# Optimization experiments

Hardware: AMD Instinct MI355X
Metric: run time of the kernel (lower is better)

The kernel has to match this reference:

```python
import jax, jax.numpy as jnp
import numpy as np

K, D, N = 32, 64, 65536
LOG_2PI = float(np.log(2.0 * np.pi))


def setup_inputs() -> dict:
    key = jax.random.key(0)
    k1, k2, k3, k4 = jax.random.split(key, 4)
    X = jax.random.normal(k1, (N, D), dtype=jnp.float32)
    loc = jax.random.normal(k2, (K, D), dtype=jnp.float32)
    # SPD full covariances per component: A A^T + I
    A = 0.1 * jax.random.normal(k3, (K, D, D), dtype=jnp.float32)
    cov = jnp.einsum('kij,klj->kil', A, A) + jnp.eye(D, dtype=jnp.float32)
    pi = jax.random.normal(k4, (K,), dtype=jnp.float32)
    return {"X": X, "loc": loc, "cov": cov, "pi": pi}


def _gmm_log_prob(X, loc, cov, pi):
    d = X.shape[-1]
    L = jnp.linalg.cholesky(cov)                       # [K, d, d]
    diff = X[:, None, :] - loc[None, :, :]             # [N, K, d]
    # per-component triangular solve: z_k = L_k^{-1} (x - mu_k)
    solve = lambda Lk, dk: jax.scipy.linalg.solve_triangular(Lk, dk.T, lower=True)  # [d, N]
    z = jax.vmap(solve, in_axes=(0, 1))(L, diff)       # [K, d, N]
    maha = jnp.sum(z * z, axis=1).T                    # [N, K]
    half_logdet = jnp.sum(jnp.log(jnp.diagonal(L, axis1=-2, axis2=-1)), axis=-1)  # [K]
    comp_logp = -0.5 * (d * LOG_2PI + maha) - half_logdet[None, :]  # [N, K]
    # Categorical(softmax(pi)).logits followed by log_softmax == log_softmax(pi)
    weighted = comp_logp + jax.nn.log_softmax(pi)[None, :]
    return jax.scipy.special.logsumexp(weighted, axis=1, keepdims=True)  # [N, 1]


def reference(X, loc, cov, pi):
    return _gmm_log_prob(X, loc, cov, pi)
```

## Files before the change

kernel.cpp:

```cpp
#include <hip/hip_runtime.h>
#include <math.h>

#define KCOMP 32
#define DDIM 64
#define LOG_2PI 1.8378770664093453f

#define WFRAG_HALF8S 64
#define WCOMP_BYTES 10240

typedef _Float16 half8 __attribute__((ext_vector_type(8)));
typedef float floatx16 __attribute__((ext_vector_type(16)));
typedef float float2v __attribute__((ext_vector_type(2)));

__device__ inline float rdlane(float v, int l) {
    return __uint_as_float(__builtin_amdgcn_readlane(__float_as_uint(v), l));
}

template <int J>
__device__ __forceinline__ void fused_step(float (&Srow)[DDIM], float2v (&LM)[DDIM],
                                           float& mydiag, const int t) {
    constexpr int NPAD = ((J + 7) / 8) * 8;
    float2v am[8];
    #pragma unroll
    for (int e = 0; e < 8; ++e) am[e] = (float2v){0.f, 0.f};
    #pragma unroll
    for (int p8 = 0; p8 < NPAD; p8 += 8) {
        float b[8];
        #pragma unroll
        for (int e = 0; e < 8; ++e) b[e] = rdlane(LM[p8 + e].x, J);
        #pragma unroll
        for (int e = 0; e < 8; ++e) {
            float2v bb = {b[e], b[e]};
            am[e] += LM[p8 + e] * bb;
        }
    }
    float2v red = ((am[0] + am[1]) + (am[2] + am[3]))
                + ((am[4] + am[5]) + (am[6] + am[7]));
    float dot = red.x;
    float ms  = red.y;
    float v  = Srow[J] - dot;
    float dj = rdlane(v, J);
    float r  = rsqrtf(dj);
    r = r * (1.5f - 0.5f * dj * r * r);
    float lv = (t >= J) ? v * r : 0.f;
    float mv = (t < J) ? (-ms * r) : ((t == J) ? r : 0.f);
    LM[J] = (float2v){lv, mv};
    if (t == J) mydiag = dj;
}

template <int J>
__device__ __forceinline__ void fused_run(float (&Srow)[DDIM], float2v (&LM)[DDIM],
                                          float& mydiag, const int t) {
    fused_step<J>(Srow, LM, mydiag, t);
    if constexpr (J + 1 < DDIM) fused_run<J + 1>(Srow, LM, mydiag, t);
}

__global__ __launch_bounds__(64, 1) void gmm_prep(const float* __restrict__ loc,
                                                  const float* __restrict__ cov,
                                                  const float* __restrict__ pi,
                                                  _Float16* __restrict__ wt,
                                                  float* __restrict__ cstout)
{
    const int k = blockIdx.x;
    const int t = threadIdx.x;

    __shared__ float M[DDIM][DDIM + 1];
    __shared__ float mu_s[DDIM];

    float Srow[DDIM];
    float2v LM[DDIM];

    {
        const float4* Sg = (const float4*)(cov + (size_t)k * DDIM * DDIM + (size_t)t * DDIM);
        #pragma unroll
        for (int q = 0; q < DDIM / 4; ++q) {
            float4 v = Sg[q];
            Srow[q * 4 + 0] = v.x; Srow[q * 4 + 1] = v.y;
            Srow[q * 4 + 2] = v.z; Srow[q * 4 + 3] = v.w;
        }
    }
    #pragma unroll
    for (int i = 0; i < DDIM; ++i) LM[i] = (float2v){0.f, 0.f};
    mu_s[t] = loc[k * DDIM + t];

    float mydiag = 1.f;
    fused_run<0>(Srow, LM, mydiag, t);

    float hld;
    {
        float lg = 0.5f * logf(mydiag);
        #pragma unroll
        for (int w = 1; w < 64; w <<= 1) lg += __shfl_xor(lg, w);
        hld = lg;
    }

    #pragma unroll
    for (int i = 0; i < DDIM; ++i) M[i][t] = LM[i].y;
    __syncthreads();

    float bt = 0.f;
    #pragma unroll 4
    for (int j = 0; j < DDIM; ++j) bt += M[t][j] * mu_s[j];

    {
        const int r = t >> 5, lrow = t & 31;
        half8* wp = (half8*)wt;
        const size_t fbase = ((size_t)k * 2 + r) * 5;
        #pragma unroll
        for (int c = 0; c < 8; ++c) {
            half8 v;
            #pragma unroll
            for (int e = 0; e < 8; ++e) v[e] = (_Float16)M[t][c * 8 + e];
            int fl = lrow + 32 * (c & 1);
            wp[(fbase + (c >> 1)) * WFRAG_HALF8S + fl] = v;
        }
        {
            float nb = -bt;
            _Float16 h0 = (_Float16)nb;
            _Float16 h1 = (_Float16)(nb - (float)h0);
            half8 v;
            #pragma unroll
            for (int e = 0; e < 8; ++e) v[e] = (_Float16)0.f;
            v[0] = h0; v[1] = h1;
            wp[(fbase + 4) * WFRAG_HALF8S + lrow] = v;
        }
        {
            half8 v;
            #pragma unroll
            for (int e = 0; e < 8; ++e) v[e] = (_Float16)0.f;
            wp[(fbase + 4) * WFRAG_HALF8S + lrow + 32] = v;
        }
    }

    if (t == 0) {
        float mxp = pi[0];
        for (int i = 1; i < KCOMP; ++i) mxp = fmaxf(mxp, pi[i]);
        float s = 0.f;
        for (int i = 0; i < KCOMP; ++i) s += __expf(pi[i] - mxp);
        float lse = mxp + logf(s);
        cstout[k] = (pi[k] - lse) - hld - 0.5f * (float)DDIM * LOG_2PI;
    }
}

__global__ __launch_bounds__(256, 1) void gmm_main(const float* __restrict__ X,
                                                   const _Float16* __restrict__ wt,
                                                   const float* __restrict__ cst,
                                                   float* __restrict__ out)
{
    __shared__ float2 part[4][128];

    const int tid  = threadIdx.x;
    const int wave = tid >> 6;
    const int lane = tid & 63;
    const int col  = lane & 31;
    const int h    = lane >> 5;
    const int ptbase = blockIdx.x * 128;

    half8 bf[4][5];
    #pragma unroll
    for (int g = 0; g < 4; ++g) {
        const float* xr = X + (size_t)(ptbase + g * 32 + col) * DDIM;
        #pragma unroll
        for (int s = 0; s < 4; ++s) {
            int c = s * 2 + h;
            float4 lo = *(const float4*)(xr + c * 8);
            float4 hi = *(const float4*)(xr + c * 8 + 4);
            half8 v;
            v[0] = (_Float16)lo.x; v[1] = (_Float16)lo.y;
            v[2] = (_Float16)lo.z; v[3] = (_Float16)lo.w;
            v[4] = (_Float16)hi.x; v[5] = (_Float16)hi.y;
            v[6] = (_Float16)hi.z; v[7] = (_Float16)hi.w;
            bf[g][s] = v;
        }
        half8 v;
        #pragma unroll
        for (int e = 0; e < 8; ++e) v[e] = (_Float16)0.f;
        if (h == 0) { v[0] = (_Float16)1.f; v[1] = (_Float16)1.f; }
        bf[g][4] = v;
    }

    const half8* wp = (const half8*)wt;
    const int comp0 = wave * 8;

    float mx[4], sm[4];
    #pragma unroll
    for (int g = 0; g < 4; ++g) { mx[g] = -INFINITY; sm[g] = 0.f; }

    half8 wfA[5], wfB[5];
    #pragma unroll
    for (int s = 0; s < 5; ++s)
        wfA[s] = wp[((size_t)comp0 * 2 + 0) * 5 * WFRAG_HALF8S + s * WFRAG_HALF8S + lane];

    #pragma unroll 1
    for (int q = 0; q < 8; ++q) {
        const int c = comp0 + q;

        #pragma unroll
        for (int s = 0; s < 5; ++s)
            wfB[s] = wp[((size_t)c * 2 + 1) * 5 * WFRAG_HALF8S + s * WFRAG_HALF8S + lane];

        float sP[4];

        {
            floatx16 a0 = {0.f}, a1 = {0.f}, a2 = {0.f}, a3 = {0.f};
            #pragma unroll
            for (int s = 0; s < 5; ++s) {
                a0 = __builtin_amdgcn_mfma_f32_32x32x16_f16(wfA[s], bf[0][s], a0, 0, 0, 0);
                a1 = __builtin_amdgcn_mfma_f32_32x32x16_f16(wfA[s], bf[1][s], a1, 0, 0, 0);
                a2 = __builtin_amdgcn_mfma_f32_32x32x16_f16(wfA[s], bf[2][s], a2, 0, 0, 0);
                a3 = __builtin_amdgcn_mfma_f32_32x32x16_f16(wfA[s], bf[3][s], a3, 0, 0, 0);
            }
            float p0 = 0.f, p1 = 0.f, p2 = 0.f, p3 = 0.f;
            #pragma unroll
            for (int r = 0; r < 16; ++r) {
                p0 += a0[r] * a0[r]; p1 += a1[r] * a1[r];
                p2 += a2[r] * a2[r]; p3 += a3[r] * a3[r];
            }
            sP[0] = p0; sP[1] = p1; sP[2] = p2; sP[3] = p3;
        }

        if (q < 7) {
            #pragma unroll
            for (int s = 0; s < 5; ++s)
                wfA[s] = wp[((size_t)(c + 1) * 2 + 0) * 5 * WFRAG_HALF8S + s * WFRAG_HALF8S + lane];
        }

        {
            floatx16 a0 = {0.f}, a1 = {0.f}, a2 = {0.f}, a3 = {0.f};
            #pragma unroll
            for (int s = 0; s < 5; ++s) {
                a0 = __builtin_amdgcn_mfma_f32_32x32x16_f16(wfB[s], bf[0][s], a0, 0, 0, 0);
                a1 = __builtin_amdgcn_mfma_f32_32x32x16_f16(wfB[s], bf[1][s], a1, 0, 0, 0);
                a2 = __builtin_amdgcn_mfma_f32_32x32x16_f16(wfB[s], bf[2][s], a2, 0, 0, 0);
                a3 = __builtin_amdgcn_mfma_f32_32x32x16_f16(wfB[s], bf[3][s], a3, 0, 0, 0);
            }
            float p0 = 0.f, p1 = 0.f, p2 = 0.f, p3 = 0.f;
            #pragma unroll
            for (int r = 0; r < 16; ++r) {
                p0 += a0[r] * a0[r]; p1 += a1[r] * a1[r];
                p2 += a2[r] * a2[r]; p3 += a3[r] * a3[r];
            }
            sP[0] += p0; sP[1] += p1; sP[2] += p2; sP[3] += p3;
        }

        const float ck = cst[c];
        #pragma unroll
        for (int g = 0; g < 4; ++g) {
            float sfull = sP[g] + __shfl_xor(sP[g], 32);
            float lp = ck - 0.5f * sfull;
            float nm = fmaxf(mx[g], lp);
            sm[g] = sm[g] * __expf(mx[g] - nm) + __expf(lp - nm);
            mx[g] = nm;
        }
    }

    if (h == 0) {
        #pragma unroll
        for (int g = 0; g < 4; ++g)
            part[wave][g * 32 + col] = make_float2(mx[g], sm[g]);
    }
    __syncthreads();

    if (tid < 128) {
        float2 p0 = part[0][tid], p1 = part[1][tid];
        float2 p2 = part[2][tid], p3 = part[3][tid];
        float m = fmaxf(fmaxf(p0.x, p1.x), fmaxf(p2.x, p3.x));
        float s = p0.y * __expf(p0.x - m) + p1.y * __expf(p1.x - m)
                + p2.y * __expf(p2.x - m) + p3.y * __expf(p3.x - m);
        out[ptbase + tid] = m + logf(s);
    }
}

extern "C" void kernel_launch(void* const* d_in, const int* in_sizes, int n_in,
                              void* d_out, int out_size, void* d_ws, size_t ws_size,
                              hipStream_t stream) {
    const float* X   = (const float*)d_in[0];
    const float* loc = (const float*)d_in[1];
    const float* cov = (const float*)d_in[2];
    const float* pi  = (const float*)d_in[3];
    float* out = (float*)d_out;

    char* ws = (char*)d_ws;
    _Float16* wt = (_Float16*)ws;
    float* cstp  = (float*)(ws + (size_t)KCOMP * WCOMP_BYTES);

    const int n = in_sizes[0] / DDIM;

    gmm_prep<<<KCOMP, 64, 0, stream>>>(loc, cov, pi, wt, cstp);
    gmm_main<<<n / 128, 256, 0, stream>>>(X, wt, cstp, out);
}
```

Measured before the change: 45.87 us.

## Split Cholesky-inverse prep across eight waves with LDS partial-sum reduction

The per-component Cholesky/inverse prep kernel goes from one 64-thread wave to 512 threads (8 waves). Each wave owns every eighth column of L and M, computes a partial dot product, and the partials are combined through double-buffered shared memory with a barrier each step. This shortens the serial dependency chain per step and cuts register pressure (8 columns per thread instead of 64), at the cost of 64 block-wide barriers and LDS traffic. The Newton refinement of rsqrt is dropped.

```diff
diff --git a/kernel.cpp b/kernel.cpp
--- a/kernel.cpp
+++ b/kernel.cpp
@@ -17,58 +17,67 @@
 }
 
 template <int J>
-__device__ __forceinline__ void fused_step(float (&Srow)[DDIM], float2v (&LM)[DDIM],
-                                           float& mydiag, const int t) {
-    constexpr int NPAD = ((J + 7) / 8) * 8;
-    float2v am[8];
-    #pragma unroll
-    for (int e = 0; e < 8; ++e) am[e] = (float2v){0.f, 0.f};
-    #pragma unroll
-    for (int p8 = 0; p8 < NPAD; p8 += 8) {
-        float b[8];
-        #pragma unroll
-        for (int e = 0; e < 8; ++e) b[e] = rdlane(LM[p8 + e].x, J);
-        #pragma unroll
-        for (int e = 0; e < 8; ++e) {
-            float2v bb = {b[e], b[e]};
-            am[e] += LM[p8 + e] * bb;
-        }
-    }
-    float2v red = ((am[0] + am[1]) + (am[2] + am[3]))
-                + ((am[4] + am[5]) + (am[6] + am[7]));
-    float dot = red.x;
-    float ms  = red.y;
-    float v  = Srow[J] - dot;
+__device__ __forceinline__ void fused_step(const float (&Srow)[DDIM], float2v (&LM)[8],
+                                           float2v* __restrict__ pbuf, float& mydiag,
+                                           const int t, const int g) {
+    float b[8];
+    #pragma unroll
+    for (int e = 0; e < 8; ++e) b[e] = rdlane(LM[e].x, J);
+    float2v am0 = {0.f, 0.f}, am1 = {0.f, 0.f}, am2 = {0.f, 0.f}, am3 = {0.f, 0.f};
+    #pragma unroll
+    for (int e = 0; e < 8; ++e) {
+        float2v bb = {b[e], b[e]};
+        switch (e & 3) {
+            case 0: am0 += LM[e] * bb; break;
+            case 1: am1 += LM[e] * bb; break;
+            case 2: am2 += LM[e] * bb; break;
+            default: am3 += LM[e] * bb; break;
+        }
+    }
+    float2v part = (am0 + am1) + (am2 + am3);
+    float2v* slot = pbuf + (J & 1) * 512;
+    slot[g * 64 + t] = part;
+    __syncthreads();
+    float2v red = ((slot[0 * 64 + t] + slot[1 * 64 + t]) + (slot[2 * 64 + t] + slot[3 * 64 + t]))
+                + ((slot[4 * 64 + t] + slot[5 * 64 + t]) + (slot[6 * 64 + t] + slot[7 * 64 + t]));
+    float v  = Srow[J] - red.x;
     float dj = rdlane(v, J);
     float r  = rsqrtf(dj);
-    r = r * (1.5f - 0.5f * dj * r * r);
-    float lv = (t >= J) ? v * r : 0.f;
-    float mv = (t < J) ? (-ms * r) : ((t == J) ? r : 0.f);
-    LM[J] = (float2v){lv, mv};
-    if (t == J) mydiag = dj;
+    if (g == (J & 7)) {
+        constexpr int I = J >> 3;
+        float lv = (t >= J) ? v * r : 0.f;
+        float mv = (t < J) ? (-red.y * r) : ((t == J) ? r : 0.f);
+        LM[I] = (float2v){lv, mv};
+        if (t == J) mydiag = dj;
+    }
 }
 
 template <int J>
-__device__ __forceinline__ void fused_run(float (&Srow)[DDIM], float2v (&LM)[DDIM],
-                                          float& mydiag, const int t) {
-    fused_step<J>(Srow, LM, mydiag, t);
-    if constexpr (J + 1 < DDIM) fused_run<J + 1>(Srow, LM, mydiag, t);
-}
-
-__global__ __launch_bounds__(64, 1) void gmm_prep(const float* __restrict__ loc,
-                                                  const float* __restrict__ cov,
-                                                  const float* __restrict__ pi,
-                                                  _Float16* __restrict__ wt,
-                                                  float* __restrict__ cstout)
+__device__ __forceinline__ void fused_run(const float (&Srow)[DDIM], float2v (&LM)[8],
+                                          float2v* __restrict__ pbuf, float& mydiag,
+                                          const int t, const int g) {
+    fused_step<J>(Srow, LM, pbuf, mydiag, t, g);
+    if constexpr (J + 1 < DDIM) fused_run<J + 1>(Srow, LM, pbuf, mydiag, t, g);
+}
+
+__global__ __launch_bounds__(512, 1) void gmm_prep(const float* __restrict__ loc,
+                                                   const float* __restrict__ cov,
+                                                   const float* __restrict__ pi,
+                                                   _Float16* __restrict__ wt,
+                                                   float* __restrict__ cstout)
 {
-    const int k = blockIdx.x;
-    const int t = threadIdx.x;
-
-    __shared__ float M[DDIM][DDIM + 1];
+    const int k   = blockIdx.x;
+    const int tid = threadIdx.x;
+    const int g   = tid >> 6;
+    const int t   = tid & 63;
+
+    __shared__ float2v pbuf[2 * 512];
+    __shared__ float Mlds[DDIM][DDIM + 1];
     __shared__ float mu_s[DDIM];
+    __shared__ float hpart[8];
 
     float Srow[DDIM];
-    float2v LM[DDIM];
+    float2v LM[8];
 
     {
         const float4* Sg = (const float4*)(cov + (size_t)k * DDIM * DDIM + (size_t)t * DDIM);
@@ -80,29 +89,27 @@
         }
     }
     #pragma unroll
-    for (int i = 0; i < DDIM; ++i) LM[i] = (float2v){0.f, 0.f};
-    mu_s[t] = loc[k * DDIM + t];
+    for (int i = 0; i < 8; ++i) LM[i] = (float2v){0.f, 0.f};
+    if (tid < DDIM) mu_s[tid] = loc[k * DDIM + tid];
 
     float mydiag = 1.f;
-    fused_run<0>(Srow, LM, mydiag, t);
-
-    float hld;
+    fused_run<0>(Srow, LM, pbuf, mydiag, t, g);
+
     {
         float lg = 0.5f * logf(mydiag);
         #pragma unroll
         for (int w = 1; w < 64; w <<= 1) lg += __shfl_xor(lg, w);
-        hld = lg;
-    }
-
-    #pragma unroll
-    for (int i = 0; i < DDIM; ++i) M[i][t] = LM[i].y;
+        if (t == 0) hpart[g] = lg;
+    }
+    #pragma unroll
+    for (int i = 0; i < 8; ++i) Mlds[g + 8 * i][t] = LM[i].y;
     __syncthreads();
 
-    float bt = 0.f;
-    #pragma unroll 4
-    for (int j = 0; j < DDIM; ++j) bt += M[t][j] * mu_s[j];
-
-    {
+    if (tid < 64) {
+        float bt = 0.f;
+        #pragma unroll 4
+        for (int j = 0; j < DDIM; ++j) bt += Mlds[t][j] * mu_s[j];
+
         const int r = t >> 5, lrow = t & 31;
         half8* wp = (half8*)wt;
         const size_t fbase = ((size_t)k * 2 + r) * 5;
@@ -110,7 +117,7 @@
         for (int c = 0; c < 8; ++c) {
             half8 v;
             #pragma unroll
-            for (int e = 0; e < 8; ++e) v[e] = (_Float16)M[t][c * 8 + e];
+            for (int e = 0; e < 8; ++e) v[e] = (_Float16)Mlds[t][c * 8 + e];
             int fl = lrow + 32 * (c & 1);
             wp[(fbase + (c >> 1)) * WFRAG_HALF8S + fl] = v;
         }
@@ -130,15 +137,17 @@
             for (int e = 0; e < 8; ++e) v[e] = (_Float16)0.f;
             wp[(fbase + 4) * WFRAG_HALF8S + lrow + 32] = v;
         }
-    }
-
-    if (t == 0) {
-        float mxp = pi[0];
-        for (int i = 1; i < KCOMP; ++i) mxp = fmaxf(mxp, pi[i]);
-        float s = 0.f;
-        for (int i = 0; i < KCOMP; ++i) s += __expf(pi[i] - mxp);
-        float lse = mxp + logf(s);
-        cstout[k] = (pi[k] - lse) - hld - 0.5f * (float)DDIM * LOG_2PI;
+
+        if (tid == 0) {
+            float hld = ((hpart[0] + hpart[1]) + (hpart[2] + hpart[3]))
+                      + ((hpart[4] + hpart[5]) + (hpart[6] + hpart[7]));
+            float mxp = pi[0];
+            for (int i = 1; i < KCOMP; ++i) mxp = fmaxf(mxp, pi[i]);
+            float s = 0.f;
+            for (int i = 0; i < KCOMP; ++i) s += __expf(pi[i] - mxp);
+            float lse = mxp + logf(s);
+            cstout[k] = (pi[k] - lse) - hld - 0.5f * (float)DDIM * LOG_2PI;
+        }
     }
 }
 
@@ -286,6 +295,6 @@
 
     const int n = in_sizes[0] / DDIM;
 
-    gmm_prep<<<KCOMP, 64, 0, stream>>>(loc, cov, pi, wt, cstp);
+    gmm_prep<<<KCOMP, 512, 0, stream>>>(loc, cov, pi, wt, cstp);
     gmm_main<<<n / 128, 256, 0, stream>>>(X, wt, cstp, out);
 }
```

New measurement: 55.77 us. +21.6%, slower.
